# Optimization experiments

Hardware: AMD Instinct MI355X
Metric: run time of the kernel (lower is better)

## Reference

```python
import jax, jax.numpy as jnp
import numpy as np

DIM = 1024
N_HEAD = 16
HEAD_DIM = DIM // N_HEAD


def setup_inputs() -> dict:
    key = jax.random.key(0)
    ks = jax.random.split(key, 5)
    scale = 0.02
    x = jax.random.normal(ks[0], (4, 2048, DIM), dtype=jnp.float32)
    W_qkv = jax.random.normal(ks[1], (DIM, 3 * DIM), dtype=jnp.float32) * scale
    b_qkv = jnp.zeros((3 * DIM,), dtype=jnp.float32)
    W_proj = jax.random.normal(ks[2], (DIM, DIM), dtype=jnp.float32) * scale
    b_proj = jnp.zeros((DIM,), dtype=jnp.float32)
    return {"x": x, "W_qkv": W_qkv, "b_qkv": b_qkv, "W_proj": W_proj, "b_proj": b_proj}


def reference(x, W_qkv, b_qkv, W_proj, b_proj):
    B, N, C = x.shape
    qkv = x @ W_qkv + b_qkv                       # [B,N,3C]
    qkv = qkv.reshape(B, N, 3, N_HEAD, HEAD_DIM)
    q, k, v = qkv[:, :, 0], qkv[:, :, 1], qkv[:, :, 2]   # [B,N,H,d]
    # scores: [B,H,N,N]
    att = jnp.einsum('bnhd,bmhd->bhnm', q, k) * (1.0 / np.sqrt(HEAD_DIM))
    att = jax.nn.softmax(att, axis=-1)
    out = jnp.einsum('bhnm,bmhd->bnhd', att, v).reshape(B, N, C)
    return out @ W_proj + b_proj
```

## Files before the change

kernel.cpp:

```cpp
#include <hip/hip_runtime.h>
#include <stdint.h>

#define DEV __device__ __forceinline__

typedef __bf16 bf16x8 __attribute__((ext_vector_type(8)));
typedef float f32x4 __attribute__((ext_vector_type(4)));
typedef float f32x16 __attribute__((ext_vector_type(16)));

DEV uint16_t f2bf(float f) {
  union { float f; uint32_t u; } v; v.f = f;
  return (uint16_t)((v.u + 0x7FFFu + ((v.u >> 16) & 1u)) >> 16);
}
DEV float bf2f(uint16_t b) {
  union { uint32_t u; float f; } v; v.u = (uint32_t)b << 16;
  return v.f;
}

#define GLD_LDS(gsrc, ldst)                                                   \
  __builtin_amdgcn_global_load_lds(                                           \
      (__attribute__((address_space(1))) void*)(void*)(gsrc),                 \
      (__attribute__((address_space(3))) void*)(ldst), 16, 0, 0)

__global__ __launch_bounds__(256) void k_conv_x(const float* __restrict__ in,
                                                uint16_t* __restrict__ out,
                                                int n8) {
  int i = blockIdx.x * 256 + threadIdx.x;
  if (i >= n8) return;
  const float4* p = (const float4*)in;
  float4 a = p[i * 2], b = p[i * 2 + 1];
  union { uint16_t s[8]; uint4 v; } o;
  o.s[0] = f2bf(a.x); o.s[1] = f2bf(a.y); o.s[2] = f2bf(a.z); o.s[3] = f2bf(a.w);
  o.s[4] = f2bf(b.x); o.s[5] = f2bf(b.y); o.s[6] = f2bf(b.z); o.s[7] = f2bf(b.w);
  ((uint4*)out)[i] = o.v;
}

__global__ __launch_bounds__(256) void k_transpose_w(const float* __restrict__ in,
                                                     uint16_t* __restrict__ out,
                                                     int K, int Ncols) {
  __shared__ float tile[32][33];
  int n0 = blockIdx.x * 32, k0 = blockIdx.y * 32;
  int tx = threadIdx.x & 31, ty = threadIdx.x >> 5;
  #pragma unroll
  for (int r = ty; r < 32; r += 8)
    tile[r][tx] = in[(size_t)(k0 + r) * Ncols + n0 + tx];
  __syncthreads();
  #pragma unroll
  for (int r = ty; r < 32; r += 8)
    out[(size_t)(n0 + r) * K + k0 + tx] = f2bf(tile[tx][r]);
}

template <int MODE>
__global__ __launch_bounds__(256) void k_gemm(
    const uint16_t* __restrict__ A, const uint16_t* __restrict__ BT,
    const float* __restrict__ bias, float* __restrict__ fout, int Ndim,
    uint16_t* __restrict__ qb, uint16_t* __restrict__ kb,
    uint16_t* __restrict__ vtb) {
  __shared__ uint16_t As[2][128 * 32];
  __shared__ uint16_t Bs[2][128 * 32];
  const int K = 1024;
  int tid = threadIdx.x;
  int lane = tid & 63, wid = tid >> 6;
  int lg = lane >> 4, lr = lane & 15;
  int wr = wid >> 1, wc = wid & 1;
  int bm = blockIdx.x, bn = blockIdx.y;

  int c0 = tid, c1 = tid + 256;
  int r0 = c0 >> 2, sl0 = (c0 & 3) ^ (r0 & 3);
  int r1 = c1 >> 2, sl1 = (c1 & 3) ^ (r1 & 3);
  const uint16_t* gA0 = A + (size_t)(bm * 128 + r0) * K + sl0 * 8;
  const uint16_t* gA1 = A + (size_t)(bm * 128 + r1) * K + sl1 * 8;
  const uint16_t* gB0 = BT + (size_t)(bn * 128 + r0) * K + sl0 * 8;
  const uint16_t* gB1 = BT + (size_t)(bn * 128 + r1) * K + sl1 * 8;

  uint32_t aoff[4], boff[4];
  #pragma unroll
  for (int i = 0; i < 4; ++i) {
    int rowa = wr * 64 + i * 16 + lr;
    aoff[i] = rowa * 64 + ((lg ^ (rowa & 3)) << 4);
    int rowb = wc * 64 + i * 16 + lr;
    boff[i] = rowb * 64 + ((lg ^ (rowb & 3)) << 4);
  }

  f32x4 acc[4][4] = {};

  auto stageg = [&](int ks, int buf) {
    int ko = ks * 32;
    GLD_LDS(gA0 + ko, &As[buf][wid * 512]);
    GLD_LDS(gA1 + ko, &As[buf][2048 + wid * 512]);
    GLD_LDS(gB0 + ko, &Bs[buf][wid * 512]);
    GLD_LDS(gB1 + ko, &Bs[buf][2048 + wid * 512]);
  };

  auto gbody = [&](int cur, int ksn, bool dostage) {
    if (dostage) stageg(ksn, cur ^ 1);
    const char* Ab = (const char*)As + cur * 8192;
    const char* Bb = (const char*)Bs + cur * 8192;
    bf16x8 af[4], bfv[4];
    #pragma unroll
    for (int i = 0; i < 4; ++i) af[i] = *(const bf16x8*)(Ab + aoff[i]);
    #pragma unroll
    for (int j = 0; j < 4; ++j) bfv[j] = *(const bf16x8*)(Bb + boff[j]);
    __builtin_amdgcn_s_setprio(1);
    #pragma unroll
    for (int i = 0; i < 4; ++i)
      #pragma unroll
      for (int j = 0; j < 4; ++j)
        acc[i][j] = __builtin_amdgcn_mfma_f32_16x16x32_bf16(af[i], bfv[j],
                                                            acc[i][j], 0, 0, 0);
    __builtin_amdgcn_s_setprio(0);
    __syncthreads();
  };

  stageg(0, 0);
  __syncthreads();
  for (int ks = 0; ks < 30; ks += 2) {
    gbody(0, ks + 1, true);
    gbody(1, ks + 2, true);
  }
  gbody(0, 31, true);
  gbody(1, 0, false);

  int m0 = bm * 128 + wr * 64;
  int n0 = bn * 128 + wc * 64;
  if (MODE == 1) {
    #pragma unroll
    for (int i = 0; i < 4; ++i) {
      int row = m0 + i * 16 + lg * 4;
      #pragma unroll
      for (int j = 0; j < 4; ++j) {
        int col = n0 + j * 16 + lr;
        float bv = bias[col];
        #pragma unroll
        for (int r = 0; r < 4; ++r)
          fout[(size_t)(row + r) * Ndim + col] = acc[i][j][r] + bv;
      }
    }
  } else {
    #pragma unroll
    for (int i = 0; i < 4; ++i) {
      int rowb = m0 + i * 16 + lg * 4;
      int b = rowb >> 11, t = rowb & 2047;
      #pragma unroll
      for (int j = 0; j < 4; ++j) {
        int colb = n0 + j * 16 + lr;
        int which = colb >> 10;
        int hd = colb & 1023;
        int h = hd >> 6, d = hd & 63;
        float bv = bias[colb];
        size_t bh = (size_t)(b * 16 + h);
        if (which == 2) {
          union { uint16_t s[4]; uint2 v; } pk;
          #pragma unroll
          for (int r = 0; r < 4; ++r) pk.s[r] = f2bf(acc[i][j][r] + bv);
          *(uint2*)&vtb[(bh * 64 + d) * 2048 + t] = pk.v;
        } else {
          uint16_t* dst = which ? kb : qb;
          #pragma unroll
          for (int r = 0; r < 4; ++r)
            dst[(bh * 2048 + t + r) * 64 + d] = f2bf(acc[i][j][r] + bv);
        }
      }
    }
  }
}

__global__ __launch_bounds__(256) void k_attn(const uint16_t* __restrict__ qb,
                                              const uint16_t* __restrict__ kb,
                                              const uint16_t* __restrict__ vtb,
                                              uint16_t* __restrict__ ob) {
  __shared__ uint16_t SM[4][64 * 64];
  int tid = threadIdx.x, lane = tid & 63, wid = tid >> 6;
  int l31 = lane & 31, hi = lane >> 5;
  int rx = (l31 & 7) ^ (((l31 >> 3) & 3) << 1);
  int bid = blockIdx.x;
  int bh = (bid & 7) * 8 + ((bid >> 3) & 7);
  int qt = bid >> 6;
  const uint16_t* qbh = qb + (size_t)bh * 2048 * 64;
  const uint16_t* kbh = kb + (size_t)bh * 2048 * 64;
  const uint16_t* vbh = vtb + (size_t)bh * 64 * 2048;
  int q = qt * 128 + wid * 32 + l31;

  uint32_t koff[8];
  #pragma unroll
  for (int kvt = 0; kvt < 2; ++kvt)
    #pragma unroll
    for (int ks = 0; ks < 4; ++ks)
      koff[kvt * 4 + ks] = (kvt * 32 + l31) * 128 + (((ks * 2 + hi) ^ rx) << 4);

  const float QSC = 0.18033688011112042f;
  bf16x8 qf[4];
  #pragma unroll
  for (int ks = 0; ks < 4; ++ks) {
    union { uint16_t s[8]; bf16x8 v; uint4 u; } ti, to;
    ti.u = *(const uint4*)(qbh + (size_t)q * 64 + ks * 16 + hi * 8);
    #pragma unroll
    for (int e = 0; e < 8; ++e) to.s[e] = f2bf(bf2f(ti.s[e]) * QSC);
    qf[ks] = to.v;
  }

  f32x16 ovt[2] = {};
  float lrow = 0.f;

  int r0 = tid >> 3;
  int sx = (tid & 7) ^ (r0 & 7) ^ (((r0 >> 3) & 3) << 1);
  int r1 = r0 + 32;

  auto stage = [&](int kt, int buf) {
    uint16_t* KN = &SM[buf][0];
    uint16_t* VN = &SM[2 + buf][0];
    GLD_LDS(kbh + (size_t)(kt * 64 + r0) * 64 + sx * 8, KN + wid * 512);
    GLD_LDS(kbh + (size_t)(kt * 64 + r1) * 64 + sx * 8, KN + 2048 + wid * 512);
    GLD_LDS(vbh + (size_t)r0 * 2048 + kt * 64 + sx * 8, VN + wid * 512);
    GLD_LDS(vbh + (size_t)r1 * 2048 + kt * 64 + sx * 8, VN + 2048 + wid * 512);
  };

  auto body = [&](int cur, int ktn, bool dostage) {
    if (dostage) stage(ktn, cur ^ 1);
    const char* Kc = (const char*)SM + cur * 8192;
    const char* Vc = (const char*)SM + 16384 + cur * 8192;

    f32x16 sv[2] = {};
    __builtin_amdgcn_s_setprio(1);
    #pragma unroll
    for (int kvt = 0; kvt < 2; ++kvt)
      #pragma unroll
      for (int ks = 0; ks < 4; ++ks) {
        bf16x8 kf = *(const bf16x8*)(Kc + koff[kvt * 4 + ks]);
        sv[kvt] = __builtin_amdgcn_mfma_f32_32x32x16_bf16(kf, qf[ks], sv[kvt], 0, 0, 0);
      }
    __builtin_amdgcn_s_setprio(0);

    float ps0 = 0.f, ps1 = 0.f, ps2 = 0.f, ps3 = 0.f;
    #pragma unroll
    for (int t = 0; t < 2; ++t)
      #pragma unroll
      for (int r = 0; r < 16; r += 4) {
        float p0 = __builtin_amdgcn_exp2f(sv[t][r + 0]);
        float p1 = __builtin_amdgcn_exp2f(sv[t][r + 1]);
        float p2 = __builtin_amdgcn_exp2f(sv[t][r + 2]);
        float p3 = __builtin_amdgcn_exp2f(sv[t][r + 3]);
        sv[t][r + 0] = p0; sv[t][r + 1] = p1;
        sv[t][r + 2] = p2; sv[t][r + 3] = p3;
        ps0 += p0; ps1 += p1; ps2 += p2; ps3 += p3;
      }
    lrow += (ps0 + ps1) + (ps2 + ps3);

    union PB { uint32_t w[4]; bf16x8 v; } pb[4];
    #pragma unroll
    for (int t = 0; t < 2; ++t)
      #pragma unroll
      for (int s = 0; s < 2; ++s) {
        int rb = s * 8;
        #pragma unroll
        for (int i = 0; i < 2; ++i) {
          uint32_t a, b;
          asm("v_cvt_pk_bf16_f32 %0, %1, %2"
              : "=v"(a) : "v"(sv[t][rb + 2 * i]), "v"(sv[t][rb + 2 * i + 1]));
          asm("v_cvt_pk_bf16_f32 %0, %1, %2"
              : "=v"(b) : "v"(sv[t][rb + 4 + 2 * i]), "v"(sv[t][rb + 4 + 2 * i + 1]));
          asm("v_permlane32_swap_b32 %0, %1" : "+v"(a), "+v"(b));
          pb[2 * t + s].w[i] = a;
          pb[2 * t + s].w[2 + i] = b;
        }
      }

    __builtin_amdgcn_s_setprio(1);
    #pragma unroll
    for (int dt = 0; dt < 2; ++dt)
      #pragma unroll
      for (int ks = 0; ks < 4; ++ks) {
        bf16x8 vf = *(const bf16x8*)(Vc + koff[dt * 4 + ks]);
        ovt[dt] = __builtin_amdgcn_mfma_f32_32x32x16_bf16(vf, pb[ks].v, ovt[dt], 0, 0, 0);
      }
    __builtin_amdgcn_s_setprio(0);

    __syncthreads();
  };

  stage(0, 0);
  __syncthreads();
  for (int t = 0; t < 30; t += 2) {
    body(0, t + 1, true);
    body(1, t + 2, true);
  }
  body(0, 31, true);
  body(1, 0, false);

  lrow += __shfl_xor(lrow, 32);
  float inv = 1.f / lrow;
  int b = bh >> 4, h = bh & 15;
  size_t base = ((size_t)b * 2048 + q) * 1024 + h * 64;
  #pragma unroll
  for (int dt = 0; dt < 2; ++dt)
    #pragma unroll
    for (int r = 0; r < 16; r += 2) {
      int d = dt * 32 + (r & 3) + 8 * (r >> 2) + 4 * hi;
      uint32_t w = (uint32_t)f2bf(ovt[dt][r] * inv) |
                   ((uint32_t)f2bf(ovt[dt][r + 1] * inv) << 16);
      *(uint32_t*)&ob[base + d] = w;
    }
}

extern "C" void kernel_launch(void* const* d_in, const int* in_sizes, int n_in,
                              void* d_out, int out_size, void* d_ws,
                              size_t ws_size, hipStream_t stream) {
  const float* x = (const float*)d_in[0];
  const float* Wqkv = (const float*)d_in[1];
  const float* bqkv = (const float*)d_in[2];
  const float* Wproj = (const float*)d_in[3];
  const float* bproj = (const float*)d_in[4];
  float* out = (float*)d_out;
  char* ws = (char*)d_ws;

  uint16_t* xb = (uint16_t*)(ws);
  uint16_t* wqkvt = (uint16_t*)(ws + (16ull << 20));
  uint16_t* wprojt = (uint16_t*)(ws + (22ull << 20));
  uint16_t* qbuf = (uint16_t*)(ws + (24ull << 20));
  uint16_t* kbuf = (uint16_t*)(ws + (40ull << 20));
  uint16_t* vtb = (uint16_t*)(ws + (56ull << 20));
  uint16_t* ob = xb;

  k_conv_x<<<4096, 256, 0, stream>>>(x, xb, 1048576);
  k_transpose_w<<<dim3(96, 32), 256, 0, stream>>>(Wqkv, wqkvt, 1024, 3072);
  k_transpose_w<<<dim3(32, 32), 256, 0, stream>>>(Wproj, wprojt, 1024, 1024);
  k_gemm<0><<<dim3(64, 24), 256, 0, stream>>>(xb, wqkvt, bqkv, nullptr, 3072,
                                              qbuf, kbuf, vtb);
  k_attn<<<1024, 256, 0, stream>>>(qbuf, kbuf, vtb, ob);
  k_gemm<1><<<dim3(64, 8), 256, 0, stream>>>(ob, wprojt, bproj, out, 1024,
                                             nullptr, nullptr, nullptr);
}
```

Before: 201.6 us.

## Prefetch two tiles ahead with explicit vmcnt waits in GEMM and attention loops

Both the GEMM and attention main loops now issue loads for two K/V (or A/B) tiles up front. Each iteration waits with a partial s_waitcnt vmcnt and a raw s_barrier, computes on the current buffer, then refills that same buffer with the tile two steps ahead. This replaces the full __syncthreads pattern, which waited on all outstanding loads, so global-to-LDS copies can overlap more compute. The softmax row-sum is also switched to packed v_pk_add_f32 reductions. Relying on raw barriers and hand-counted vmcnt risks ordering bugs if the count of loads per stage changes.

Result: slower. 213.7 us (+6.0%).

```diff
diff --git a/kernel.cpp b/kernel.cpp
--- a/kernel.cpp
+++ b/kernel.cpp
@@ -4,6 +4,7 @@
 #define DEV __device__ __forceinline__
 
 typedef __bf16 bf16x8 __attribute__((ext_vector_type(8)));
+typedef float f32x2 __attribute__((ext_vector_type(2)));
 typedef float f32x4 __attribute__((ext_vector_type(4)));
 typedef float f32x16 __attribute__((ext_vector_type(16)));
 
@@ -14,12 +15,21 @@
 DEV float bf2f(uint16_t b) {
   union { uint32_t u; float f; } v; v.u = (uint32_t)b << 16;
   return v.f;
+}
+
+DEV f32x2 pkadd(f32x2 a, f32x2 b) {
+  f32x2 d;
+  asm("v_pk_add_f32 %0, %1, %2" : "=v"(d) : "v"(a), "v"(b));
+  return d;
 }
 
 #define GLD_LDS(gsrc, ldst)                                                   \
   __builtin_amdgcn_global_load_lds(                                           \
       (__attribute__((address_space(1))) void*)(void*)(gsrc),                 \
       (__attribute__((address_space(3))) void*)(ldst), 16, 0, 0)
+
+#define VMCNT(n) asm volatile("s_waitcnt vmcnt(" #n ")" ::: "memory")
+#define SBAR() asm volatile("s_barrier" ::: "memory")
 
 __global__ __launch_bounds__(256) void k_conv_x(const float* __restrict__ in,
                                                 uint16_t* __restrict__ out,
@@ -91,8 +101,7 @@
     GLD_LDS(gB1 + ko, &Bs[buf][2048 + wid * 512]);
   };
 
-  auto gbody = [&](int cur, int ksn, bool dostage) {
-    if (dostage) stageg(ksn, cur ^ 1);
+  auto gcompute = [&](int cur) {
     const char* Ab = (const char*)As + cur * 8192;
     const char* Bb = (const char*)Bs + cur * 8192;
     bf16x8 af[4], bfv[4];
@@ -108,17 +117,20 @@
         acc[i][j] = __builtin_amdgcn_mfma_f32_16x16x32_bf16(af[i], bfv[j],
                                                             acc[i][j], 0, 0, 0);
     __builtin_amdgcn_s_setprio(0);
-    __syncthreads();
   };
 
   stageg(0, 0);
-  __syncthreads();
-  for (int ks = 0; ks < 30; ks += 2) {
-    gbody(0, ks + 1, true);
-    gbody(1, ks + 2, true);
-  }
-  gbody(0, 31, true);
-  gbody(1, 0, false);
+  stageg(1, 1);
+  for (int ks = 0; ks < 30; ++ks) {
+    int cur = ks & 1;
+    VMCNT(4);
+    SBAR();
+    gcompute(cur);
+    SBAR();
+    stageg(ks + 2, cur);
+  }
+  VMCNT(4); SBAR(); gcompute(0);
+  VMCNT(0); SBAR(); gcompute(1);
 
   int m0 = bm * 128 + wr * 64;
   int n0 = bn * 128 + wc * 64;
@@ -199,7 +211,7 @@
   }
 
   f32x16 ovt[2] = {};
-  float lrow = 0.f;
+  f32x2 lr2 = {0.f, 0.f};
 
   int r0 = tid >> 3;
   int sx = (tid & 7) ^ (r0 & 7) ^ (((r0 >> 3) & 3) << 1);
@@ -214,8 +226,7 @@
     GLD_LDS(vbh + (size_t)r1 * 2048 + kt * 64 + sx * 8, VN + 2048 + wid * 512);
   };
 
-  auto body = [&](int cur, int ktn, bool dostage) {
-    if (dostage) stage(ktn, cur ^ 1);
+  auto body = [&](int cur) {
     const char* Kc = (const char*)SM + cur * 8192;
     const char* Vc = (const char*)SM + 16384 + cur * 8192;
 
@@ -230,20 +241,18 @@
       }
     __builtin_amdgcn_s_setprio(0);
 
-    float ps0 = 0.f, ps1 = 0.f, ps2 = 0.f, ps3 = 0.f;
     #pragma unroll
     for (int t = 0; t < 2; ++t)
       #pragma unroll
-      for (int r = 0; r < 16; r += 4) {
-        float p0 = __builtin_amdgcn_exp2f(sv[t][r + 0]);
-        float p1 = __builtin_amdgcn_exp2f(sv[t][r + 1]);
-        float p2 = __builtin_amdgcn_exp2f(sv[t][r + 2]);
-        float p3 = __builtin_amdgcn_exp2f(sv[t][r + 3]);
-        sv[t][r + 0] = p0; sv[t][r + 1] = p1;
-        sv[t][r + 2] = p2; sv[t][r + 3] = p3;
-        ps0 += p0; ps1 += p1; ps2 += p2; ps3 += p3;
-      }
-    lrow += (ps0 + ps1) + (ps2 + ps3);
+      for (int r = 0; r < 16; ++r) sv[t][r] = __builtin_amdgcn_exp2f(sv[t][r]);
+
+    union SX { f32x16 v; f32x2 p[8]; } u0, u1;
+    u0.v = sv[0]; u1.v = sv[1];
+    f32x2 s0 = pkadd(pkadd(pkadd(u0.p[0], u0.p[1]), pkadd(u0.p[2], u0.p[3])),
+                     pkadd(pkadd(u0.p[4], u0.p[5]), pkadd(u0.p[6], u0.p[7])));
+    f32x2 s1 = pkadd(pkadd(pkadd(u1.p[0], u1.p[1]), pkadd(u1.p[2], u1.p[3])),
+                     pkadd(pkadd(u1.p[4], u1.p[5]), pkadd(u1.p[6], u1.p[7])));
+    lr2 = pkadd(lr2, pkadd(s0, s1));
 
     union PB { uint32_t w[4]; bf16x8 v; } pb[4];
     #pragma unroll
@@ -273,19 +282,22 @@
         ovt[dt] = __builtin_amdgcn_mfma_f32_32x32x16_bf16(vf, pb[ks].v, ovt[dt], 0, 0, 0);
       }
     __builtin_amdgcn_s_setprio(0);
-
-    __syncthreads();
   };
 
   stage(0, 0);
-  __syncthreads();
-  for (int t = 0; t < 30; t += 2) {
-    body(0, t + 1, true);
-    body(1, t + 2, true);
-  }
-  body(0, 31, true);
-  body(1, 0, false);
-
+  stage(1, 1);
+  for (int t = 0; t < 30; ++t) {
+    int cur = t & 1;
+    VMCNT(4);
+    SBAR();
+    body(cur);
+    SBAR();
+    stage(t + 2, cur);
+  }
+  VMCNT(4); SBAR(); body(0);
+  VMCNT(0); SBAR(); body(1);
+
+  float lrow = lr2.x + lr2.y;
   lrow += __shfl_xor(lrow, 32);
   float inv = 1.f / lrow;
   int b = bh >> 4, h = bh & 15;
```
